# Kernel optimization log

Measured on AMD Instinct MI355X. Metric: run time of the kernel, lower is better.

## Reference

```python
import jax, jax.numpy as jnp
import numpy as np


def setup_inputs() -> dict:
    key = jax.random.key(0)
    k1, k2, k3, k4 = jax.random.split(key, 4)
    B, S, E, H = 8, 2048, 1024, 64
    x = jax.random.normal(k1, (B, S, E), dtype=jnp.float32)
    scale = 1.0 / np.sqrt(E)
    Wq = jax.random.normal(k2, (E, H), dtype=jnp.float32) * scale
    Wk = jax.random.normal(k3, (E, H), dtype=jnp.float32) * scale
    Wv = jax.random.normal(k4, (E, H), dtype=jnp.float32) * scale
    return {"x": x, "Wq": Wq, "Wk": Wk, "Wv": Wv}


def reference(x, Wq, Wk, Wv):
    # x: [B, S, E]; Wq/Wk/Wv: [E, H]
    B, S, E = x.shape
    H = Wq.shape[1]
    q = x @ Wq  # [B, S, H]
    k = x @ Wk
    v = x @ Wv
    inv_sqrt_h = 1.0 / jnp.sqrt(jnp.asarray(H, dtype=x.dtype))
    att = jnp.einsum("bqh,bkh->bqk", q, k) * inv_sqrt_h  # [B, S, S]
    causal = jnp.tril(jnp.ones((S, S), dtype=bool))
    att = jnp.where(causal, att, jnp.asarray(-jnp.inf, dtype=att.dtype))
    att = jax.nn.softmax(att, axis=-1)
    # dropout p=0.0 (eval) -> identity
    return jnp.einsum("bqk,bkh->bqh", att, v)  # [B, S, H]
```

## Files before the change

### kernel.cpp

```cpp
#include <hip/hip_runtime.h>
#include <math.h>

typedef __attribute__((ext_vector_type(8))) short bf16x8;
typedef __attribute__((ext_vector_type(16))) float fx16;

#define SEQ 2048
#define HD 64

__device__ __forceinline__ unsigned f2bf_bits(float f){
  unsigned u = __float_as_uint(f);
  return (u + 0x7fffu + ((u >> 16) & 1u)) >> 16;
}
__device__ __forceinline__ unsigned cvt_pk_bf16(float a, float b){
  unsigned r;
  asm("v_cvt_pk_bf16_f32 %0, %1, %2" : "=v"(r) : "v"(a), "v"(b));
  return r;
}
union U8 { bf16x8 v; short s[8]; unsigned u[4]; };

__device__ __forceinline__ fx16 mfma_bf16(bf16x8 a, bf16x8 b, fx16 c){
  return __builtin_amdgcn_mfma_f32_32x32x16_bf16(a, b, c, 0, 0, 0);
}
__device__ __forceinline__ fx16 fzero(){
  fx16 z;
#pragma unroll
  for (int i = 0; i < 16; ++i) z[i] = 0.f;
  return z;
}

__global__ __launch_bounds__(256) void wconv_kernel(
    const float* __restrict__ Wq, const float* __restrict__ Wk, const float* __restrict__ Wv,
    short* __restrict__ wth, short* __restrict__ wtl)
{
  int n = blockIdx.x;
  int mat = n >> 6, col = n & 63;
  const float* W = (mat == 0) ? Wq : (mat == 1) ? Wk : Wv;
  for (int k = threadIdx.x; k < 1024; k += 256) {
    float f = W[(size_t)k * 64 + col];
    unsigned hb = f2bf_bits(f);
    float hf = __uint_as_float(hb << 16);
    unsigned lb = f2bf_bits(f - hf);
    wth[(size_t)n * 1024 + k] = (short)hb;
    wtl[(size_t)n * 1024 + k] = (short)lb;
  }
}

__global__ __launch_bounds__(256) void proj_kernel(
    const float* __restrict__ x, const short* __restrict__ wth, const short* __restrict__ wtl,
    short* __restrict__ qh, short* __restrict__ ql,
    short* __restrict__ kh, short* __restrict__ kl,
    short* __restrict__ vth, short* __restrict__ vtl)
{
  __shared__ short Xs[64 * 128];
  __shared__ short Ws[192 * 128];
  __shared__ float Vb[64 * 68];

  const int tid = threadIdx.x;
  const int lane = tid & 63, w = tid >> 6;
  const int l31 = lane & 31, h = lane >> 5;
  const int m = w & 1;
  const int nset = (w >> 1) * 3;
  const int row0 = blockIdx.x * 64;

  fx16 accP[3], accQ[3];
#pragma unroll
  for (int t = 0; t < 3; ++t) { accP[t] = fzero(); accQ[t] = fzero(); }

  const int xrow = tid >> 2;
  const int xkc = (tid & 3) * 16;
  const int xswz = (xrow & 7) << 4;

  for (int k0 = 0; k0 < 1024; k0 += 64) {
    float xf[16];
    {
      float4 a = *(const float4*)(x + (size_t)(row0 + xrow) * 1024 + k0 + xkc + 0);
      float4 b = *(const float4*)(x + (size_t)(row0 + xrow) * 1024 + k0 + xkc + 4);
      float4 c = *(const float4*)(x + (size_t)(row0 + xrow) * 1024 + k0 + xkc + 8);
      float4 d = *(const float4*)(x + (size_t)(row0 + xrow) * 1024 + k0 + xkc + 12);
      xf[0]=a.x; xf[1]=a.y; xf[2]=a.z; xf[3]=a.w;
      xf[4]=b.x; xf[5]=b.y; xf[6]=b.z; xf[7]=b.w;
      xf[8]=c.x; xf[9]=c.y; xf[10]=c.z; xf[11]=c.w;
      xf[12]=d.x; xf[13]=d.y; xf[14]=d.z; xf[15]=d.w;
    }
    U8 xh0, xh1, xl0, xl1;
#pragma unroll
    for (int i = 0; i < 16; ++i) {
      unsigned hb = f2bf_bits(xf[i]);
      float hf = __uint_as_float(hb << 16);
      unsigned lb = f2bf_bits(xf[i] - hf);
      if (i < 8) { xh0.s[i] = (short)hb; xl0.s[i] = (short)lb; }
      else       { xh1.s[i - 8] = (short)hb; xl1.s[i - 8] = (short)lb; }
    }
    {
      char* rp = (char*)Xs + xrow * 256;
      *(bf16x8*)(rp + (( 2 * xkc      ) ^ xswz)) = xh0.v;
      *(bf16x8*)(rp + (( 2 * xkc + 16 ) ^ xswz)) = xh1.v;
      *(bf16x8*)(rp + 128 + (( 2 * xkc      ) ^ xswz)) = xl0.v;
      *(bf16x8*)(rp + 128 + (( 2 * xkc + 16 ) ^ xswz)) = xl1.v;
    }
#pragma unroll
    for (int jj = 0; jj < 12; ++jj) {
      int idx = jj * 256 + tid;
      int wrow = idx >> 4, slot = idx & 15;
      int half = slot >> 3, sb = (slot & 7) << 4;
      int srcb = sb ^ ((wrow & 7) << 4);
      const short* src = (half ? wtl : wth) + (size_t)wrow * 1024 + k0 + (srcb >> 1);
      bf16x8 v = *(const bf16x8*)src;
      *(bf16x8*)((char*)Ws + wrow * 256 + half * 128 + sb) = v;
    }
    __syncthreads();
#pragma unroll
    for (int ks = 0; ks < 4; ++ks) {
      const char* arow = (const char*)Xs + (m * 32 + l31) * 256;
      const int sw = (l31 & 7) << 4;
      const int kb = ks * 32 + 16 * h;
      bf16x8 ah = *(const bf16x8*)(arow + (kb ^ sw));
      bf16x8 al = *(const bf16x8*)(arow + 128 + (kb ^ sw));
#pragma unroll
      for (int t = 0; t < 3; ++t) {
        int n = (nset + t) * 32 + l31;
        const char* brow = (const char*)Ws + n * 256;
        const int swb = (n & 7) << 4;
        bf16x8 bh = *(const bf16x8*)(brow + (kb ^ swb));
        bf16x8 bl = *(const bf16x8*)(brow + 128 + (kb ^ swb));
        accP[t] = mfma_bf16(ah, bh, accP[t]);
        accQ[t] = mfma_bf16(ah, bl, accQ[t]);
        accQ[t] = mfma_bf16(al, bh, accQ[t]);
      }
    }
    __syncthreads();
  }

#pragma unroll
  for (int t = 0; t < 3; ++t) {
    int nt = nset + t;
    int mat = nt >> 1;
    int colb = (nt & 1) * 32 + l31;
    if (mat < 2) {
      short* dh = (mat == 0) ? qh : kh;
      short* dl = (mat == 0) ? ql : kl;
#pragma unroll
      for (int r = 0; r < 16; ++r) {
        float f = accP[t][r] + accQ[t][r];
        int rowg = row0 + m * 32 + (r & 3) + 8 * (r >> 2) + 4 * h;
        unsigned hb = f2bf_bits(f);
        float hf = __uint_as_float(hb << 16);
        unsigned lb = f2bf_bits(f - hf);
        dh[(size_t)rowg * 64 + colb] = (short)hb;
        dl[(size_t)rowg * 64 + colb] = (short)lb;
      }
    } else {
#pragma unroll
      for (int r = 0; r < 16; ++r) {
        float f = accP[t][r] + accQ[t][r];
        int srel = m * 32 + (r & 3) + 8 * (r >> 2) + 4 * h;
        Vb[srel * 68 + (nt - 4) * 32 + l31] = f;
      }
    }
  }
  __syncthreads();
  {
    int d = tid >> 2, sc = (tid & 3) * 16;
    int b = row0 >> 11, s0 = row0 & 2047;
    U8 hv0, hv1, lv0, lv1;
#pragma unroll
    for (int ss = 0; ss < 16; ++ss) {
      float f = Vb[(sc + ss) * 68 + d];
      unsigned hb = f2bf_bits(f);
      float hf = __uint_as_float(hb << 16);
      unsigned lb = f2bf_bits(f - hf);
      if (ss < 8) { hv0.s[ss] = (short)hb; lv0.s[ss] = (short)lb; }
      else        { hv1.s[ss - 8] = (short)hb; lv1.s[ss - 8] = (short)lb; }
    }
    size_t o = (size_t)(b * 64 + d) * 2048 + s0 + sc;
    *(bf16x8*)(vth + o) = hv0.v;  *(bf16x8*)(vth + o + 8) = hv1.v;
    *(bf16x8*)(vtl + o) = lv0.v;  *(bf16x8*)(vtl + o + 8) = lv1.v;
  }
}

__global__ __launch_bounds__(256, 2) void attn_kernel(
    const short* __restrict__ qh, const short* __restrict__ ql,
    const short* __restrict__ kh, const short* __restrict__ kl,
    const short* __restrict__ vth, const short* __restrict__ vtl,
    float* __restrict__ segO, float* __restrict__ segL, float* __restrict__ segM)
{
  __shared__ short Kbuf[2][64 * 128];
  __shared__ short Vbuf[2][64 * 128];
  __shared__ float Red[2][64];

  const int bid = blockIdx.x;
  const int b = bid / 80;
  int j = bid % 80;
  int g4 = (j < 8) ? 0 : ((j < 24) ? 1 : ((j < 48) ? 2 : 3));
  int base4 = (g4 == 0) ? 0 : (g4 == 1) ? 8 : (g4 == 2) ? 24 : 48;
  int within = j - base4;
  int nch = g4 + 1;
  int qt = g4 * 8 + within / nch;
  int ch = within - (within / nch) * nch;
  int S = qt + 1, bs = S / nch, rem = S - bs * nch;
  int nsteps = bs + (ch < rem ? 1 : 0);
  int kt0 = ch * bs + (ch < rem ? ch : rem);

  const int tid = threadIdx.x;
  const int lane = tid & 63, w = tid >> 6;
  const int mk = w >> 1, nq = w & 1;
  const int l31 = lane & 31, h = lane >> 5;

  bf16x8 qf[2][4];
  {
    size_t qrow = ((size_t)b * 2048 + qt * 64 + nq * 32 + l31) * 64;
#pragma unroll
    for (int ds = 0; ds < 4; ++ds) {
      qf[0][ds] = *(const bf16x8*)(qh + qrow + ds * 16 + 8 * h);
      qf[1][ds] = *(const bf16x8*)(ql + qrow + ds * 16 + 8 * h);
    }
  }

  const int slot = tid & 15;
  const int half = slot >> 3;
  const int sb = (slot & 7) << 4;
  const int rbase = tid >> 4;
  const int d0 = (sb ^ ((rbase & 7) << 4)) >> 1;
  const short* ksrc = half ? kl : kh;
  const short* vsrc = half ? vtl : vth;
  const int woff = rbase * 256 + half * 128 + sb;

  fx16 stA, stB, stC, accA0, accA1, accB0, accB1;
  accA0 = fzero(); accA1 = fzero(); accB0 = fzero(); accB1 = fzero();
  float Mrun = -3e38f, lrun = 0.f;

  bf16x8 kreg[4], vreg[4];
#pragma unroll
  for (int jj = 0; jj < 4; ++jj) {
    kreg[jj] = *(const bf16x8*)(ksrc + ((size_t)b * 2048 + (size_t)kt0 * 64 + rbase + 16 * jj) * 64 + d0);
    vreg[jj] = *(const bf16x8*)(vsrc + ((size_t)(b * 64 + rbase + 16 * jj)) * 2048 + kt0 * 64 + d0);
  }
#pragma unroll
  for (int jj = 0; jj < 4; ++jj) {
    *(bf16x8*)((char*)Kbuf[0] + woff + jj * 4096) = kreg[jj];
    *(bf16x8*)((char*)Vbuf[0] + woff + jj * 4096) = vreg[jj];
  }
  __syncthreads();

  for (int it = 0; it < nsteps; ++it) {
    const int kt = kt0 + it;
    const int p = it & 1;
    const bool hasnext = (it + 1 < nsteps);
    if (hasnext) {
      int kn = kt + 1;
#pragma unroll
      for (int jj = 0; jj < 4; ++jj) {
        kreg[jj] = *(const bf16x8*)(ksrc + ((size_t)b * 2048 + (size_t)kn * 64 + rbase + 16 * jj) * 64 + d0);
        vreg[jj] = *(const bf16x8*)(vsrc + ((size_t)(b * 64 + rbase + 16 * jj)) * 2048 + kn * 64 + d0);
      }
    }
    stA = fzero(); stB = fzero(); stC = fzero();
    {
      const char* arow = (const char*)Kbuf[p] + (mk * 32 + l31) * 256;
      const int sw = (l31 & 7) << 4;
#pragma unroll
      for (int ds = 0; ds < 4; ++ds) {
        const int kb = ds * 32 + 16 * h;
        bf16x8 ah = *(const bf16x8*)(arow + (kb ^ sw));
        bf16x8 al = *(const bf16x8*)(arow + 128 + (kb ^ sw));
        stA = mfma_bf16(ah, qf[0][ds], stA);
        stB = mfma_bf16(ah, qf[1][ds], stB);
        stC = mfma_bf16(al, qf[0][ds], stC);
      }
    }
    float sv[16];
#pragma unroll
    for (int r = 0; r < 16; ++r) {
      float s = (stA[r] + stB[r] + stC[r]) * 0.125f;
      if (kt == qt) {
        int krel = (r & 3) + 8 * (r >> 2) + 4 * h;
        if (mk * 32 + krel > nq * 32 + l31) s = -3e38f;
      }
      sv[r] = s;
    }
    float tm = sv[0];
#pragma unroll
    for (int r = 1; r < 16; ++r) tm = fmaxf(tm, sv[r]);
    tm = fmaxf(tm, __shfl_xor(tm, 32, 64));
    if (lane < 32) Red[mk][nq * 32 + l31] = tm;
    __syncthreads();
    float om = Red[mk ^ 1][nq * 32 + l31];
    if (hasnext) {
#pragma unroll
      for (int jj = 0; jj < 4; ++jj) {
        *(bf16x8*)((char*)Kbuf[p ^ 1] + woff + jj * 4096) = kreg[jj];
        *(bf16x8*)((char*)Vbuf[p ^ 1] + woff + jj * 4096) = vreg[jj];
      }
    }
    float Mnew = fmaxf(fmaxf(tm, om), Mrun);
    float alpha = __expf(Mrun - Mnew);
    Mrun = Mnew;
    float pvv[16]; float psum = 0.f;
#pragma unroll
    for (int r = 0; r < 16; ++r) { pvv[r] = __expf(sv[r] - Mnew); psum += pvv[r]; }
    psum += __shfl_xor(psum, 32, 64);
    lrun = lrun * alpha + psum;
#pragma unroll
    for (int r = 0; r < 16; ++r) { accA0[r] *= alpha; accA1[r] *= alpha; accB0[r] *= alpha; accB1[r] *= alpha; }
    unsigned chv[8], clv[8];
#pragma unroll
    for (int q2 = 0; q2 < 8; ++q2) {
      unsigned c = cvt_pk_bf16(pvv[2 * q2], pvv[2 * q2 + 1]);
      chv[q2] = c;
      float f0 = __uint_as_float(c << 16);
      float f1 = __uint_as_float(c & 0xffff0000u);
      clv[q2] = cvt_pk_bf16(pvv[2 * q2] - f0, pvv[2 * q2 + 1] - f1);
    }
#pragma unroll
    for (int kp = 0; kp < 2; ++kp) {
      U8 ph, pl;
      {
        unsigned c0 = chv[4 * kp], c1 = chv[4 * kp + 1], c2 = chv[4 * kp + 2], c3 = chv[4 * kp + 3];
        unsigned x0 = (unsigned)__shfl_xor((int)c0, 32, 64);
        unsigned x1 = (unsigned)__shfl_xor((int)c1, 32, 64);
        unsigned x2 = (unsigned)__shfl_xor((int)c2, 32, 64);
        unsigned x3 = (unsigned)__shfl_xor((int)c3, 32, 64);
        ph.u[0] = h ? x2 : c0;  ph.u[1] = h ? x3 : c1;
        ph.u[2] = h ? c2 : x0;  ph.u[3] = h ? c3 : x1;
        c0 = clv[4 * kp]; c1 = clv[4 * kp + 1]; c2 = clv[4 * kp + 2]; c3 = clv[4 * kp + 3];
        x0 = (unsigned)__shfl_xor((int)c0, 32, 64);
        x1 = (unsigned)__shfl_xor((int)c1, 32, 64);
        x2 = (unsigned)__shfl_xor((int)c2, 32, 64);
        x3 = (unsigned)__shfl_xor((int)c3, 32, 64);
        pl.u[0] = h ? x2 : c0;  pl.u[1] = h ? x3 : c1;
        pl.u[2] = h ? c2 : x0;  pl.u[3] = h ? c3 : x1;
      }
      const int kbv = mk * 64 + kp * 32 + 16 * h;
      const int vsw = (l31 & 7) << 4;
#pragma unroll
      for (int md = 0; md < 2; ++md) {
        const char* vrow = (const char*)Vbuf[p] + (md * 32 + l31) * 256;
        bf16x8 vh = *(const bf16x8*)(vrow + (kbv ^ vsw));
        bf16x8 vl = *(const bf16x8*)(vrow + 128 + (kbv ^ vsw));
        if (md == 0) {
          accA0 = mfma_bf16(vh, ph.v, accA0);
          accB0 = mfma_bf16(vh, pl.v, accB0);
          accB0 = mfma_bf16(vl, ph.v, accB0);
        } else {
          accA1 = mfma_bf16(vh, ph.v, accA1);
          accB1 = mfma_bf16(vh, pl.v, accB1);
          accB1 = mfma_bf16(vl, ph.v, accB1);
        }
      }
    }
    __syncthreads();
  }

  float* o = segO + (((size_t)bid * 2 + mk) * 2 + nq) * 2048;
#pragma unroll
  for (int md = 0; md < 2; ++md) {
#pragma unroll
    for (int r = 0; r < 16; ++r) {
      int d = md * 32 + (r & 3) + 8 * (r >> 2) + 4 * h;
      float val = md ? (accA1[r] + accB1[r]) : (accA0[r] + accB0[r]);
      o[d * 32 + l31] = val;
    }
  }
  if (lane < 32) segL[((size_t)bid * 2 + mk) * 64 + nq * 32 + l31] = lrun;
  if (mk == 0 && lane < 32) segM[(size_t)bid * 64 + nq * 32 + l31] = Mrun;
}

__global__ __launch_bounds__(256) void combine_kernel(
    const float* __restrict__ segO, const float* __restrict__ segL,
    const float* __restrict__ segM, float* __restrict__ out)
{
  __shared__ float Ot[64 * 68];
  __shared__ float Ls[64];
  __shared__ float Sc[4][64];

  int bq = blockIdx.x;
  int b = bq >> 5, qt = bq & 31;
  int g4 = qt >> 3, nch = g4 + 1;
  int base4 = (g4 == 0) ? 0 : (g4 == 1) ? 8 : (g4 == 2) ? 24 : 48;
  int slot0 = b * 80 + base4 + (qt - g4 * 8) * nch;
  int tid = threadIdx.x;

  if (tid < 64) {
    float M = -3e38f;
    for (int c = 0; c < nch; ++c) M = fmaxf(M, segM[(size_t)(slot0 + c) * 64 + tid]);
    float L = 0.f;
    for (int c = 0; c < nch; ++c) {
      float s = __expf(segM[(size_t)(slot0 + c) * 64 + tid] - M);
      Sc[c][tid] = s;
      L += s * (segL[((size_t)(slot0 + c) * 2 + 0) * 64 + tid] +
                segL[((size_t)(slot0 + c) * 2 + 1) * 64 + tid]);
    }
    Ls[tid] = L;
  }
  __syncthreads();
  {
    int d = tid >> 2, q0 = (tid & 3) * 16;
    for (int qq = 0; qq < 16; ++qq) {
      int q = q0 + qq;
      float acc = 0.f;
      for (int c = 0; c < nch; ++c) {
        size_t s0 = (((size_t)(slot0 + c) * 2 + 0) * 2 + (q >> 5)) * 2048 + d * 32 + (q & 31);
        size_t s1 = (((size_t)(slot0 + c) * 2 + 1) * 2 + (q >> 5)) * 2048 + d * 32 + (q & 31);
        acc += Sc[c][q] * (segO[s0] + segO[s1]);
      }
      Ot[d * 68 + q] = acc;
    }
  }
  __syncthreads();
  {
    int q = tid >> 2, dd0 = (tid & 3) * 16;
    float inv = 1.f / Ls[q];
    float* dst = out + ((size_t)b * 2048 + qt * 64 + q) * 64 + dd0;
#pragma unroll
    for (int i = 0; i < 4; ++i) {
      float4 vv;
      vv.x = Ot[(dd0 + 4 * i + 0) * 68 + q] * inv;
      vv.y = Ot[(dd0 + 4 * i + 1) * 68 + q] * inv;
      vv.z = Ot[(dd0 + 4 * i + 2) * 68 + q] * inv;
      vv.w = Ot[(dd0 + 4 * i + 3) * 68 + q] * inv;
      *(float4*)(dst + 4 * i) = vv;
    }
  }
}

extern "C" void kernel_launch(void* const* d_in, const int* in_sizes, int n_in,
                              void* d_out, int out_size, void* d_ws, size_t ws_size,
                              hipStream_t stream) {
  const float* x  = (const float*)d_in[0];
  const float* Wq = (const float*)d_in[1];
  const float* Wk = (const float*)d_in[2];
  const float* Wv = (const float*)d_in[3];

  char* wsb = (char*)d_ws;
  short* wth = (short*)(wsb + 0);
  short* wtl = (short*)(wsb + 393216);
  short* qh  = (short*)(wsb + 786432);
  short* ql  = (short*)(wsb + 2883584);
  short* kh  = (short*)(wsb + 4980736);
  short* kl  = (short*)(wsb + 7077888);
  short* vth = (short*)(wsb + 9175040);
  short* vtl = (short*)(wsb + 11272192);
  float* segO = (float*)(wsb + 13369344);
  float* segL = (float*)(wsb + 13369344 + 20971520);
  float* segM = (float*)(wsb + 13369344 + 20971520 + 327680);

  wconv_kernel<<<192, 256, 0, stream>>>(Wq, Wk, Wv, wth, wtl);
  proj_kernel<<<256, 256, 0, stream>>>(x, wth, wtl, qh, ql, kh, kl, vth, vtl);
  attn_kernel<<<640, 256, 0, stream>>>(qh, ql, kh, kl, vth, vtl, segO, segL, segM);
  combine_kernel<<<256, 256, 0, stream>>>(segO, segL, segM, (float*)d_out);
}
```

Measured before the change: 109.3 us.

## Prepack weights in MFMA fragment order, drop LDS in projection, use 128-row attention tiles

The weight conversion kernel now writes bf16 hi/lo weights directly in per-lane MFMA fragment layout. The projection kernel loads x and weight fragments straight from global memory into registers with software double-buffering, replacing the LDS staging and block barriers. The attention kernel now gives each wave 32 queries over a full 64-key tile with a 128-query block, which removes the cross-wave max reduction through shared memory and halves the block count. The combine kernel is adapted to the new segment layout with vectorized loads. In exchange there is more register pressure, fewer blocks for load balancing, and redundant global reads of x per wave.

```diff
diff --git a/kernel.cpp b/kernel.cpp
--- a/kernel.cpp
+++ b/kernel.cpp
@@ -30,29 +30,39 @@
 
 __global__ __launch_bounds__(256) void wconv_kernel(
     const float* __restrict__ Wq, const float* __restrict__ Wk, const float* __restrict__ Wv,
-    short* __restrict__ wth, short* __restrict__ wtl)
+    short* __restrict__ wsB)
 {
-  int n = blockIdx.x;
+  int gid = blockIdx.x * 4 + (threadIdx.x >> 6);
+  int lane = threadIdx.x & 63;
+  int l31 = lane & 31, h = lane >> 5;
+  int half = gid & 1;
+  int rem = gid >> 1;
+  int t = rem % 6;
+  int stage = rem / 6;
+  int n = t * 32 + l31;
   int mat = n >> 6, col = n & 63;
   const float* W = (mat == 0) ? Wq : (mat == 1) ? Wk : Wv;
-  for (int k = threadIdx.x; k < 1024; k += 256) {
-    float f = W[(size_t)k * 64 + col];
+  int kbase = stage * 16 + h * 8;
+  U8 o;
+#pragma unroll
+  for (int i = 0; i < 8; ++i) {
+    float f = W[(size_t)(kbase + i) * 64 + col];
     unsigned hb = f2bf_bits(f);
-    float hf = __uint_as_float(hb << 16);
-    unsigned lb = f2bf_bits(f - hf);
-    wth[(size_t)n * 1024 + k] = (short)hb;
-    wtl[(size_t)n * 1024 + k] = (short)lb;
-  }
-}
-
-__global__ __launch_bounds__(256) void proj_kernel(
-    const float* __restrict__ x, const short* __restrict__ wth, const short* __restrict__ wtl,
+    if (half == 0) o.s[i] = (short)hb;
+    else {
+      float hf = __uint_as_float(hb << 16);
+      o.s[i] = (short)f2bf_bits(f - hf);
+    }
+  }
+  *(bf16x8*)(wsB + (size_t)gid * 512 + lane * 8) = o.v;
+}
+
+__global__ __launch_bounds__(256, 2) void proj_kernel(
+    const float* __restrict__ x, const short* __restrict__ wsB,
     short* __restrict__ qh, short* __restrict__ ql,
     short* __restrict__ kh, short* __restrict__ kl,
     short* __restrict__ vth, short* __restrict__ vtl)
 {
-  __shared__ short Xs[64 * 128];
-  __shared__ short Ws[192 * 128];
   __shared__ float Vb[64 * 68];
 
   const int tid = threadIdx.x;
@@ -61,75 +71,76 @@
   const int m = w & 1;
   const int nset = (w >> 1) * 3;
   const int row0 = blockIdx.x * 64;
+  const size_t xrow = (size_t)(row0 + m * 32 + l31) * 1024;
 
   fx16 accP[3], accQ[3];
 #pragma unroll
   for (int t = 0; t < 3; ++t) { accP[t] = fzero(); accQ[t] = fzero(); }
 
-  const int xrow = tid >> 2;
-  const int xkc = (tid & 3) * 16;
-  const int xswz = (xrow & 7) << 4;
-
-  for (int k0 = 0; k0 < 1024; k0 += 64) {
-    float xf[16];
-    {
-      float4 a = *(const float4*)(x + (size_t)(row0 + xrow) * 1024 + k0 + xkc + 0);
-      float4 b = *(const float4*)(x + (size_t)(row0 + xrow) * 1024 + k0 + xkc + 4);
-      float4 c = *(const float4*)(x + (size_t)(row0 + xrow) * 1024 + k0 + xkc + 8);
-      float4 d = *(const float4*)(x + (size_t)(row0 + xrow) * 1024 + k0 + xkc + 12);
-      xf[0]=a.x; xf[1]=a.y; xf[2]=a.z; xf[3]=a.w;
-      xf[4]=b.x; xf[5]=b.y; xf[6]=b.z; xf[7]=b.w;
-      xf[8]=c.x; xf[9]=c.y; xf[10]=c.z; xf[11]=c.w;
-      xf[12]=d.x; xf[13]=d.y; xf[14]=d.z; xf[15]=d.w;
-    }
-    U8 xh0, xh1, xl0, xl1;
-#pragma unroll
-    for (int i = 0; i < 16; ++i) {
-      unsigned hb = f2bf_bits(xf[i]);
-      float hf = __uint_as_float(hb << 16);
-      unsigned lb = f2bf_bits(xf[i] - hf);
-      if (i < 8) { xh0.s[i] = (short)hb; xl0.s[i] = (short)lb; }
-      else       { xh1.s[i - 8] = (short)hb; xl1.s[i - 8] = (short)lb; }
-    }
-    {
-      char* rp = (char*)Xs + xrow * 256;
-      *(bf16x8*)(rp + (( 2 * xkc      ) ^ xswz)) = xh0.v;
-      *(bf16x8*)(rp + (( 2 * xkc + 16 ) ^ xswz)) = xh1.v;
-      *(bf16x8*)(rp + 128 + (( 2 * xkc      ) ^ xswz)) = xl0.v;
-      *(bf16x8*)(rp + 128 + (( 2 * xkc + 16 ) ^ xswz)) = xl1.v;
-    }
-#pragma unroll
-    for (int jj = 0; jj < 12; ++jj) {
-      int idx = jj * 256 + tid;
-      int wrow = idx >> 4, slot = idx & 15;
-      int half = slot >> 3, sb = (slot & 7) << 4;
-      int srcb = sb ^ ((wrow & 7) << 4);
-      const short* src = (half ? wtl : wth) + (size_t)wrow * 1024 + k0 + (srcb >> 1);
-      bf16x8 v = *(const bf16x8*)src;
-      *(bf16x8*)((char*)Ws + wrow * 256 + half * 128 + sb) = v;
-    }
-    __syncthreads();
-#pragma unroll
-    for (int ks = 0; ks < 4; ++ks) {
-      const char* arow = (const char*)Xs + (m * 32 + l31) * 256;
-      const int sw = (l31 & 7) << 4;
-      const int kb = ks * 32 + 16 * h;
-      bf16x8 ah = *(const bf16x8*)(arow + (kb ^ sw));
-      bf16x8 al = *(const bf16x8*)(arow + 128 + (kb ^ sw));
-#pragma unroll
-      for (int t = 0; t < 3; ++t) {
-        int n = (nset + t) * 32 + l31;
-        const char* brow = (const char*)Ws + n * 256;
-        const int swb = (n & 7) << 4;
-        bf16x8 bh = *(const bf16x8*)(brow + (kb ^ swb));
-        bf16x8 bl = *(const bf16x8*)(brow + 128 + (kb ^ swb));
-        accP[t] = mfma_bf16(ah, bh, accP[t]);
-        accQ[t] = mfma_bf16(ah, bl, accQ[t]);
-        accQ[t] = mfma_bf16(al, bh, accQ[t]);
-      }
-    }
-    __syncthreads();
-  }
+  float4 A0[4][2], A1[4][2];
+  bf16x8 B0[6], B1[6];
+
+#define LOADA(AB, C1)                                                   \
+  {                                                                     \
+    _Pragma("unroll")                                                   \
+    for (int ks = 0; ks < 4; ++ks) {                                    \
+      int k = (C1) * 64 + ks * 16 + h * 8;                              \
+      AB[ks][0] = *(const float4*)(x + xrow + k);                       \
+      AB[ks][1] = *(const float4*)(x + xrow + k + 4);                   \
+    }                                                                   \
+  }
+
+#define LOADB(BB, SR)                                                   \
+  {                                                                     \
+    _Pragma("unroll")                                                   \
+    for (int tt = 0; tt < 3; ++tt) {                                    \
+      size_t g2 = ((size_t)(SR) * 6 + nset + tt) * 2;                   \
+      BB[tt * 2 + 0] = *(const bf16x8*)(wsB + g2 * 512 + lane * 8);     \
+      BB[tt * 2 + 1] = *(const bf16x8*)(wsB + (g2 + 1) * 512 + lane * 8);\
+    }                                                                   \
+  }
+
+#define STEP(AF, BB)                                                    \
+  {                                                                     \
+    U8 ah, al;                                                          \
+    float xf[8];                                                        \
+    xf[0] = AF[0].x; xf[1] = AF[0].y; xf[2] = AF[0].z; xf[3] = AF[0].w; \
+    xf[4] = AF[1].x; xf[5] = AF[1].y; xf[6] = AF[1].z; xf[7] = AF[1].w; \
+    _Pragma("unroll")                                                   \
+    for (int i = 0; i < 8; ++i) {                                       \
+      unsigned hb = f2bf_bits(xf[i]);                                   \
+      ah.s[i] = (short)hb;                                              \
+      float hf = __uint_as_float(hb << 16);                             \
+      al.s[i] = (short)f2bf_bits(xf[i] - hf);                           \
+    }                                                                   \
+    _Pragma("unroll")                                                   \
+    for (int tt = 0; tt < 3; ++tt) {                                    \
+      accP[tt] = mfma_bf16(ah.v, BB[tt * 2 + 0], accP[tt]);             \
+      accQ[tt] = mfma_bf16(ah.v, BB[tt * 2 + 1], accQ[tt]);             \
+      accQ[tt] = mfma_bf16(al.v, BB[tt * 2 + 0], accQ[tt]);             \
+    }                                                                   \
+  }
+
+#define CHUNK(C, ACUR, ANEXT)                                           \
+  {                                                                     \
+    if ((C) < 15) LOADA(ANEXT, (C) + 1);                                \
+    STEP(ACUR[0], B0); if ((C) * 4 + 2 < 64) LOADB(B0, (C) * 4 + 2);    \
+    STEP(ACUR[1], B1); if ((C) * 4 + 3 < 64) LOADB(B1, (C) * 4 + 3);    \
+    STEP(ACUR[2], B0); if ((C) * 4 + 4 < 64) LOADB(B0, (C) * 4 + 4);    \
+    STEP(ACUR[3], B1); if ((C) * 4 + 5 < 64) LOADB(B1, (C) * 4 + 5);    \
+  }
+
+  LOADA(A0, 0);
+  LOADB(B0, 0);
+  LOADB(B1, 1);
+  for (int c2 = 0; c2 < 8; ++c2) {
+    CHUNK(2 * c2 + 0, A0, A1);
+    CHUNK(2 * c2 + 1, A1, A0);
+  }
+#undef CHUNK
+#undef STEP
+#undef LOADB
+#undef LOADA
 
 #pragma unroll
   for (int t = 0; t < 3; ++t) {
@@ -161,7 +172,7 @@
   __syncthreads();
   {
     int d = tid >> 2, sc = (tid & 3) * 16;
-    int b = row0 >> 11, s0 = row0 & 2047;
+    int bb = row0 >> 11, s0 = row0 & 2047;
     U8 hv0, hv1, lv0, lv1;
 #pragma unroll
     for (int ss = 0; ss < 16; ++ss) {
@@ -172,7 +183,7 @@
       if (ss < 8) { hv0.s[ss] = (short)hb; lv0.s[ss] = (short)lb; }
       else        { hv1.s[ss - 8] = (short)hb; lv1.s[ss - 8] = (short)lb; }
     }
-    size_t o = (size_t)(b * 64 + d) * 2048 + s0 + sc;
+    size_t o = (size_t)(bb * 64 + d) * 2048 + s0 + sc;
     *(bf16x8*)(vth + o) = hv0.v;  *(bf16x8*)(vth + o + 8) = hv1.v;
     *(bf16x8*)(vtl + o) = lv0.v;  *(bf16x8*)(vtl + o + 8) = lv1.v;
   }
@@ -186,33 +197,32 @@
 {
   __shared__ short Kbuf[2][64 * 128];
   __shared__ short Vbuf[2][64 * 128];
-  __shared__ float Red[2][64];
 
   const int bid = blockIdx.x;
-  const int b = bid / 80;
-  int j = bid % 80;
-  int g4 = (j < 8) ? 0 : ((j < 24) ? 1 : ((j < 48) ? 2 : 3));
-  int base4 = (g4 == 0) ? 0 : (g4 == 1) ? 8 : (g4 == 2) ? 24 : 48;
-  int within = j - base4;
-  int nch = g4 + 1;
-  int qt = g4 * 8 + within / nch;
-  int ch = within - (within / nch) * nch;
-  int S = qt + 1, bs = S / nch, rem = S - bs * nch;
-  int nsteps = bs + (ch < rem ? 1 : 0);
-  int kt0 = ch * bs + (ch < rem ? ch : rem);
+  const int b = bid / 40;
+  const int j = bid % 40;
+  int qt, ch, nch;
+  if (j < 4)       { nch = 1; qt = j;               ch = 0; }
+  else if (j < 12) { nch = 2; qt = 4 + (j - 4) / 2; ch = (j - 4) % 2; }
+  else if (j < 24) { nch = 3; qt = 8 + (j - 12) / 3; ch = (j - 12) % 3; }
+  else             { nch = 4; qt = 12 + (j - 24) / 4; ch = (j - 24) % 4; }
+  const int S = 2 * qt + 2;
+  const int bs = S / nch, rem = S % nch;
+  const int nsteps = bs + (ch < rem ? 1 : 0);
+  const int kt0 = ch * bs + (ch < rem ? ch : rem);
 
   const int tid = threadIdx.x;
   const int lane = tid & 63, w = tid >> 6;
-  const int mk = w >> 1, nq = w & 1;
   const int l31 = lane & 31, h = lane >> 5;
-
-  bf16x8 qf[2][4];
+  const int qabs = qt * 128 + w * 32 + l31;
+
+  bf16x8 qf0[4], qf1[4];
   {
-    size_t qrow = ((size_t)b * 2048 + qt * 64 + nq * 32 + l31) * 64;
+    size_t qrow = ((size_t)b * 2048 + qabs) * 64;
 #pragma unroll
     for (int ds = 0; ds < 4; ++ds) {
-      qf[0][ds] = *(const bf16x8*)(qh + qrow + ds * 16 + 8 * h);
-      qf[1][ds] = *(const bf16x8*)(ql + qrow + ds * 16 + 8 * h);
+      qf0[ds] = *(const bf16x8*)(qh + qrow + ds * 16 + 8 * h);
+      qf1[ds] = *(const bf16x8*)(ql + qrow + ds * 16 + 8 * h);
     }
   }
 
@@ -225,9 +235,9 @@
   const short* vsrc = half ? vtl : vth;
   const int woff = rbase * 256 + half * 128 + sb;
 
-  fx16 stA, stB, stC, accA0, accA1, accB0, accB1;
-  accA0 = fzero(); accA1 = fzero(); accB0 = fzero(); accB1 = fzero();
+  fx16 accA0 = fzero(), accA1 = fzero(), accB0 = fzero(), accB1 = fzero();
   float Mrun = -3e38f, lrun = 0.f;
+  const int sw = (l31 & 7) << 4;
 
   bf16x8 kreg[4], vreg[4];
 #pragma unroll
@@ -254,37 +264,97 @@
         vreg[jj] = *(const bf16x8*)(vsrc + ((size_t)(b * 64 + rbase + 16 * jj)) * 2048 + kn * 64 + d0);
       }
     }
-    stA = fzero(); stB = fzero(); stC = fzero();
-    {
-      const char* arow = (const char*)Kbuf[p] + (mk * 32 + l31) * 256;
-      const int sw = (l31 & 7) << 4;
-#pragma unroll
-      for (int ds = 0; ds < 4; ++ds) {
-        const int kb = ds * 32 + 16 * h;
-        bf16x8 ah = *(const bf16x8*)(arow + (kb ^ sw));
-        bf16x8 al = *(const bf16x8*)(arow + 128 + (kb ^ sw));
-        stA = mfma_bf16(ah, qf[0][ds], stA);
-        stB = mfma_bf16(ah, qf[1][ds], stB);
-        stC = mfma_bf16(al, qf[0][ds], stC);
-      }
-    }
-    float sv[16];
-#pragma unroll
-    for (int r = 0; r < 16; ++r) {
-      float s = (stA[r] + stB[r] + stC[r]) * 0.125f;
-      if (kt == qt) {
-        int krel = (r & 3) + 8 * (r >> 2) + 4 * h;
-        if (mk * 32 + krel > nq * 32 + l31) s = -3e38f;
-      }
-      sv[r] = s;
-    }
-    float tm = sv[0];
-#pragma unroll
-    for (int r = 1; r < 16; ++r) tm = fmaxf(tm, sv[r]);
-    tm = fmaxf(tm, __shfl_xor(tm, 32, 64));
-    if (lane < 32) Red[mk][nq * 32 + l31] = tm;
-    __syncthreads();
-    float om = Red[mk ^ 1][nq * 32 + l31];
+
+#pragma unroll
+    for (int ms = 0; ms < 2; ++ms) {
+      fx16 stA = fzero(), stB = fzero(), stC = fzero();
+      {
+        const char* arow = (const char*)Kbuf[p] + (ms * 32 + l31) * 256;
+#pragma unroll
+        for (int ds = 0; ds < 4; ++ds) {
+          const int kb = ds * 32 + 16 * h;
+          bf16x8 ah = *(const bf16x8*)(arow + (kb ^ sw));
+          bf16x8 al = *(const bf16x8*)(arow + 128 + (kb ^ sw));
+          stA = mfma_bf16(ah, qf0[ds], stA);
+          stB = mfma_bf16(ah, qf1[ds], stB);
+          stC = mfma_bf16(al, qf0[ds], stC);
+        }
+      }
+      float sv[16];
+      const int kbase = kt * 64 + ms * 32;
+      const bool diag = (kbase + 31 > qt * 128 + w * 32);
+#pragma unroll
+      for (int r = 0; r < 16; ++r) {
+        float s = (stA[r] + stB[r] + stC[r]) * 0.125f;
+        if (diag) {
+          int ka = kbase + (r & 3) + 8 * (r >> 2) + 4 * h;
+          if (ka > qabs) s = -3e38f;
+        }
+        sv[r] = s;
+      }
+      float tm = sv[0];
+#pragma unroll
+      for (int r = 1; r < 16; ++r) tm = fmaxf(tm, sv[r]);
+      tm = fmaxf(tm, __shfl_xor(tm, 32, 64));
+      float Mnew = fmaxf(Mrun, tm);
+      float alpha = __expf(Mrun - Mnew);
+      Mrun = Mnew;
+      float pvv[16]; float psum = 0.f;
+#pragma unroll
+      for (int r = 0; r < 16; ++r) { pvv[r] = __expf(sv[r] - Mnew); psum += pvv[r]; }
+      psum += __shfl_xor(psum, 32, 64);
+      lrun = lrun * alpha + psum;
+#pragma unroll
+      for (int r = 0; r < 16; ++r) {
+        accA0[r] *= alpha; accA1[r] *= alpha; accB0[r] *= alpha; accB1[r] *= alpha;
+      }
+      unsigned chv[8], clv[8];
+#pragma unroll
+      for (int q2 = 0; q2 < 8; ++q2) {
+        unsigned c = cvt_pk_bf16(pvv[2 * q2], pvv[2 * q2 + 1]);
+        chv[q2] = c;
+        float f0 = __uint_as_float(c << 16);
+        float f1 = __uint_as_float(c & 0xffff0000u);
+        clv[q2] = cvt_pk_bf16(pvv[2 * q2] - f0, pvv[2 * q2 + 1] - f1);
+      }
+#pragma unroll
+      for (int kp = 0; kp < 2; ++kp) {
+        U8 ph, pl;
+        {
+          unsigned c0 = chv[4 * kp], c1 = chv[4 * kp + 1], c2 = chv[4 * kp + 2], c3 = chv[4 * kp + 3];
+          unsigned x0 = (unsigned)__shfl_xor((int)c0, 32, 64);
+          unsigned x1 = (unsigned)__shfl_xor((int)c1, 32, 64);
+          unsigned x2 = (unsigned)__shfl_xor((int)c2, 32, 64);
+          unsigned x3 = (unsigned)__shfl_xor((int)c3, 32, 64);
+          ph.u[0] = h ? x2 : c0;  ph.u[1] = h ? x3 : c1;
+          ph.u[2] = h ? c2 : x0;  ph.u[3] = h ? c3 : x1;
+          c0 = clv[4 * kp]; c1 = clv[4 * kp + 1]; c2 = clv[4 * kp + 2]; c3 = clv[4 * kp + 3];
+          x0 = (unsigned)__shfl_xor((int)c0, 32, 64);
+          x1 = (unsigned)__shfl_xor((int)c1, 32, 64);
+          x2 = (unsigned)__shfl_xor((int)c2, 32, 64);
+          x3 = (unsigned)__shfl_xor((int)c3, 32, 64);
+          pl.u[0] = h ? x2 : c0;  pl.u[1] = h ? x3 : c1;
+          pl.u[2] = h ? c2 : x0;  pl.u[3] = h ? c3 : x1;
+        }
+        const int kbv = ms * 64 + kp * 32 + 16 * h;
+#pragma unroll
+        for (int md = 0; md < 2; ++md) {
+          const char* vrow = (const char*)Vbuf[p] + (md * 32 + l31) * 256;
+          bf16x8 vh = *(const bf16x8*)(vrow + (kbv ^ sw));
+          bf16x8 vl = *(const bf16x8*)(vrow + 128 + (kbv ^ sw));
+          if (md == 0) {
+            accA0 = mfma_bf16(vh, ph.v, accA0);
+            accB0 = mfma_bf16(vh, pl.v, accB0);
+            accB0 = mfma_bf16(vl, ph.v, accB0);
+          } else {
+            accA1 = mfma_bf16(vh, ph.v, accA1);
+            accB1 = mfma_bf16(vh, pl.v, accB1);
+            accB1 = mfma_bf16(vl, ph.v, accB1);
+          }
+        }
+      }
+    }
+
     if (hasnext) {
 #pragma unroll
       for (int jj = 0; jj < 4; ++jj) {
@@ -292,133 +362,85 @@
         *(bf16x8*)((char*)Vbuf[p ^ 1] + woff + jj * 4096) = vreg[jj];
       }
     }
-    float Mnew = fmaxf(fmaxf(tm, om), Mrun);
-    float alpha = __expf(Mrun - Mnew);
-    Mrun = Mnew;
-    float pvv[16]; float psum = 0.f;
-#pragma unroll
-    for (int r = 0; r < 16; ++r) { pvv[r] = __expf(sv[r] - Mnew); psum += pvv[r]; }
-    psum += __shfl_xor(psum, 32, 64);
-    lrun = lrun * alpha + psum;
-#pragma unroll
-    for (int r = 0; r < 16; ++r) { accA0[r] *= alpha; accA1[r] *= alpha; accB0[r] *= alpha; accB1[r] *= alpha; }
-    unsigned chv[8], clv[8];
-#pragma unroll
-    for (int q2 = 0; q2 < 8; ++q2) {
-      unsigned c = cvt_pk_bf16(pvv[2 * q2], pvv[2 * q2 + 1]);
-      chv[q2] = c;
-      float f0 = __uint_as_float(c << 16);
-      float f1 = __uint_as_float(c & 0xffff0000u);
-      clv[q2] = cvt_pk_bf16(pvv[2 * q2] - f0, pvv[2 * q2 + 1] - f1);
-    }
-#pragma unroll
-    for (int kp = 0; kp < 2; ++kp) {
-      U8 ph, pl;
-      {
-        unsigned c0 = chv[4 * kp], c1 = chv[4 * kp + 1], c2 = chv[4 * kp + 2], c3 = chv[4 * kp + 3];
-        unsigned x0 = (unsigned)__shfl_xor((int)c0, 32, 64);
-        unsigned x1 = (unsigned)__shfl_xor((int)c1, 32, 64);
-        unsigned x2 = (unsigned)__shfl_xor((int)c2, 32, 64);
-        unsigned x3 = (unsigned)__shfl_xor((int)c3, 32, 64);
-        ph.u[0] = h ? x2 : c0;  ph.u[1] = h ? x3 : c1;
-        ph.u[2] = h ? c2 : x0;  ph.u[3] = h ? c3 : x1;
-        c0 = clv[4 * kp]; c1 = clv[4 * kp + 1]; c2 = clv[4 * kp + 2]; c3 = clv[4 * kp + 3];
-        x0 = (unsigned)__shfl_xor((int)c0, 32, 64);
-        x1 = (unsigned)__shfl_xor((int)c1, 32, 64);
-        x2 = (unsigned)__shfl_xor((int)c2, 32, 64);
-        x3 = (unsigned)__shfl_xor((int)c3, 32, 64);
-        pl.u[0] = h ? x2 : c0;  pl.u[1] = h ? x3 : c1;
-        pl.u[2] = h ? c2 : x0;  pl.u[3] = h ? c3 : x1;
-      }
-      const int kbv = mk * 64 + kp * 32 + 16 * h;
-      const int vsw = (l31 & 7) << 4;
-#pragma unroll
-      for (int md = 0; md < 2; ++md) {
-        const char* vrow = (const char*)Vbuf[p] + (md * 32 + l31) * 256;
-        bf16x8 vh = *(const bf16x8*)(vrow + (kbv ^ vsw));
-        bf16x8 vl = *(const bf16x8*)(vrow + 128 + (kbv ^ vsw));
-        if (md == 0) {
-          accA0 = mfma_bf16(vh, ph.v, accA0);
-          accB0 = mfma_bf16(vh, pl.v, accB0);
-          accB0 = mfma_bf16(vl, ph.v, accB0);
-        } else {
-          accA1 = mfma_bf16(vh, ph.v, accA1);
-          accB1 = mfma_bf16(vh, pl.v, accB1);
-          accB1 = mfma_bf16(vl, ph.v, accB1);
-        }
-      }
-    }
     __syncthreads();
   }
 
-  float* o = segO + (((size_t)bid * 2 + mk) * 2 + nq) * 2048;
+  float* o = segO + (size_t)bid * (64 * 128);
 #pragma unroll
   for (int md = 0; md < 2; ++md) {
 #pragma unroll
     for (int r = 0; r < 16; ++r) {
       int d = md * 32 + (r & 3) + 8 * (r >> 2) + 4 * h;
       float val = md ? (accA1[r] + accB1[r]) : (accA0[r] + accB0[r]);
-      o[d * 32 + l31] = val;
-    }
-  }
-  if (lane < 32) segL[((size_t)bid * 2 + mk) * 64 + nq * 32 + l31] = lrun;
-  if (mk == 0 && lane < 32) segM[(size_t)bid * 64 + nq * 32 + l31] = Mrun;
+      o[d * 128 + w * 32 + l31] = val;
+    }
+  }
+  if (h == 0) {
+    segL[(size_t)bid * 128 + w * 32 + l31] = lrun;
+    segM[(size_t)bid * 128 + w * 32 + l31] = Mrun;
+  }
 }
 
 __global__ __launch_bounds__(256) void combine_kernel(
     const float* __restrict__ segO, const float* __restrict__ segL,
     const float* __restrict__ segM, float* __restrict__ out)
 {
-  __shared__ float Ot[64 * 68];
-  __shared__ float Ls[64];
-  __shared__ float Sc[4][64];
-
-  int bq = blockIdx.x;
-  int b = bq >> 5, qt = bq & 31;
-  int g4 = qt >> 3, nch = g4 + 1;
-  int base4 = (g4 == 0) ? 0 : (g4 == 1) ? 8 : (g4 == 2) ? 24 : 48;
-  int slot0 = b * 80 + base4 + (qt - g4 * 8) * nch;
-  int tid = threadIdx.x;
-
-  if (tid < 64) {
+  __shared__ float Sc[4][128];
+  __shared__ float Linv[128];
+  __shared__ float Ot[64 * 132];
+
+  const int bq = blockIdx.x;
+  const int b = bq >> 4, qt = bq & 15;
+  const int g = qt >> 2, nch = g + 1;
+  const int base = (g == 0) ? qt
+                 : (g == 1) ? 4 + (qt - 4) * 2
+                 : (g == 2) ? 12 + (qt - 8) * 3
+                 : 24 + (qt - 12) * 4;
+  const int slot0 = b * 40 + base;
+  const int tid = threadIdx.x;
+
+  if (tid < 128) {
+    const int q = tid;
     float M = -3e38f;
-    for (int c = 0; c < nch; ++c) M = fmaxf(M, segM[(size_t)(slot0 + c) * 64 + tid]);
+    for (int c = 0; c < nch; ++c)
+      M = fmaxf(M, segM[(size_t)(slot0 + c) * 128 + q]);
     float L = 0.f;
     for (int c = 0; c < nch; ++c) {
-      float s = __expf(segM[(size_t)(slot0 + c) * 64 + tid] - M);
-      Sc[c][tid] = s;
-      L += s * (segL[((size_t)(slot0 + c) * 2 + 0) * 64 + tid] +
-                segL[((size_t)(slot0 + c) * 2 + 1) * 64 + tid]);
-    }
-    Ls[tid] = L;
+      float s = __expf(segM[(size_t)(slot0 + c) * 128 + q] - M);
+      Sc[c][q] = s;
+      L += s * segL[(size_t)(slot0 + c) * 128 + q];
+    }
+    Linv[q] = 1.f / L;
   }
   __syncthreads();
   {
-    int d = tid >> 2, q0 = (tid & 3) * 16;
-    for (int qq = 0; qq < 16; ++qq) {
-      int q = q0 + qq;
-      float acc = 0.f;
+    const int dr = tid >> 5;
+    const int qc = (tid & 31) * 4;
+    for (int dd = dr; dd < 64; dd += 8) {
+      float4 acc = {0.f, 0.f, 0.f, 0.f};
       for (int c = 0; c < nch; ++c) {
-        size_t s0 = (((size_t)(slot0 + c) * 2 + 0) * 2 + (q >> 5)) * 2048 + d * 32 + (q & 31);
-        size_t s1 = (((size_t)(slot0 + c) * 2 + 1) * 2 + (q >> 5)) * 2048 + d * 32 + (q & 31);
-        acc += Sc[c][q] * (segO[s0] + segO[s1]);
-      }
-      Ot[d * 68 + q] = acc;
+        float4 v = *(const float4*)(segO + (size_t)(slot0 + c) * 8192 + dd * 128 + qc);
+        acc.x += Sc[c][qc + 0] * v.x;
+        acc.y += Sc[c][qc + 1] * v.y;
+        acc.z += Sc[c][qc + 2] * v.z;
+        acc.w += Sc[c][qc + 3] * v.w;
+      }
+      *(float4*)&Ot[dd * 132 + qc] = acc;
     }
   }
   __syncthreads();
   {
-    int q = tid >> 2, dd0 = (tid & 3) * 16;
-    float inv = 1.f / Ls[q];
-    float* dst = out + ((size_t)b * 2048 + qt * 64 + q) * 64 + dd0;
-#pragma unroll
-    for (int i = 0; i < 4; ++i) {
-      float4 vv;
-      vv.x = Ot[(dd0 + 4 * i + 0) * 68 + q] * inv;
-      vv.y = Ot[(dd0 + 4 * i + 1) * 68 + q] * inv;
-      vv.z = Ot[(dd0 + 4 * i + 2) * 68 + q] * inv;
-      vv.w = Ot[(dd0 + 4 * i + 3) * 68 + q] * inv;
-      *(float4*)(dst + 4 * i) = vv;
+    const int q = tid >> 1, dh = (tid & 1) * 32;
+    const float inv = Linv[q];
+    float* dst = out + ((size_t)b * 2048 + qt * 128 + q) * 64 + dh;
+#pragma unroll
+    for (int i = 0; i < 8; ++i) {
+      float4 o;
+      o.x = Ot[(dh + 4 * i + 0) * 132 + q] * inv;
+      o.y = Ot[(dh + 4 * i + 1) * 132 + q] * inv;
+      o.z = Ot[(dh + 4 * i + 2) * 132 + q] * inv;
+      o.w = Ot[(dh + 4 * i + 3) * 132 + q] * inv;
+      *(float4*)(dst + 4 * i) = o;
     }
   }
 }
@@ -432,8 +454,7 @@
   const float* Wv = (const float*)d_in[3];
 
   char* wsb = (char*)d_ws;
-  short* wth = (short*)(wsb + 0);
-  short* wtl = (short*)(wsb + 393216);
+  short* wsB = (short*)(wsb + 0);
   short* qh  = (short*)(wsb + 786432);
   short* ql  = (short*)(wsb + 2883584);
   short* kh  = (short*)(wsb + 4980736);
@@ -441,11 +462,11 @@
   short* vth = (short*)(wsb + 9175040);
   short* vtl = (short*)(wsb + 11272192);
   float* segO = (float*)(wsb + 13369344);
-  float* segL = (float*)(wsb + 13369344 + 20971520);
-  float* segM = (float*)(wsb + 13369344 + 20971520 + 327680);
-
-  wconv_kernel<<<192, 256, 0, stream>>>(Wq, Wk, Wv, wth, wtl);
-  proj_kernel<<<256, 256, 0, stream>>>(x, wth, wtl, qh, ql, kh, kl, vth, vtl);
-  attn_kernel<<<640, 256, 0, stream>>>(qh, ql, kh, kl, vth, vtl, segO, segL, segM);
-  combine_kernel<<<256, 256, 0, stream>>>(segO, segL, segM, (float*)d_out);
-}
+  float* segL = (float*)(wsb + 23855104);
+  float* segM = (float*)(wsb + 24018944);
+
+  wconv_kernel<<<192, 256, 0, stream>>>(Wq, Wk, Wv, wsB);
+  proj_kernel<<<256, 256, 0, stream>>>(x, wsB, qh, ql, kh, kl, vth, vtl);
+  attn_kernel<<<320, 256, 0, stream>>>(qh, ql, kh, kl, vth, vtl, segO, segL, segM);
+  combine_kernel<<<128, 256, 0, stream>>>(segO, segL, segM, (float*)d_out);
+}
```

Result: faster. 99.05 us (-9.4%).
